# Optimization experiments

Measured on AMD Instinct MI355X. Metric: run time of the kernel, lower is better.

## Reference

```python
import jax, jax.numpy as jnp
import numpy as np

EPS = 0.1  # entropic regularization epsilon
N, F, R, H = 512, 32, 8, 128


def setup_inputs() -> dict:
    key = jax.random.key(0)
    ks = jax.random.split(key, 9)
    s0 = 1.0 / np.sqrt(F + R)
    sh = 1.0 / np.sqrt(H)
    return {
        "X": jax.random.normal(ks[0], (N, F), jnp.float32),
        "U": jax.random.normal(ks[1], (N, R), jnp.float32),
        "Y": jax.random.normal(ks[2], (N, R), jnp.float32),
        "Wx": jax.random.normal(ks[3], (F, H), jnp.float32) * s0,
        "Wy": jax.random.normal(ks[4], (R, H), jnp.float32) * s0,
        "b0": jnp.zeros((H,), jnp.float32),
        "W1": jax.random.normal(ks[5], (H, H), jnp.float32) * sh,
        "b1": jnp.zeros((H,), jnp.float32),
        "W2": jax.random.normal(ks[6], (H, H), jnp.float32) * sh,
        "b2": jnp.zeros((H,), jnp.float32),
        "Wout": jax.random.normal(ks[7], (H, 1), jnp.float32) * sh,
        "bout": jnp.zeros((1,), jnp.float32),
    }


def _mlp_tail(h, W1, b1, W2, b2, Wout, bout):
    h = jax.nn.softplus(h @ W1 + b1)
    h = jax.nn.softplus(h @ W2 + b2)
    return h @ Wout + bout  # [..., 1]


def reference(X, U, Y, Wx, Wy, b0, W1, b1, W2, b2, Wout, bout):
    n = X.shape[0]
    # ---- estimate_psi (potential net estimates 'y' side directly) ----
    h_row = jax.nn.softplus(X @ Wx + Y @ Wy + b0)              # [n, H]
    psi = _mlp_tail(h_row, W1, b1, W2, b2, Wout, bout)         # [n, 1]
    # ---- estimate_phi: entropic dual over all (X_i, Y_j) pairs ----
    # First-layer pre-activation built by broadcast-sum instead of concat.
    h_pair = jax.nn.softplus((X @ Wx)[:, None, :] + (Y @ Wy)[None, :, :] + b0)  # [n, n, H]
    psi_vals = _mlp_tail(h_pair, W1, b1, W2, b2, Wout, bout)[..., 0]            # [n, n]
    cost = U @ Y.T                                             # [n, n]
    slack = cost - psi_vals
    m = jnp.max(slack, axis=1, keepdims=True)                  # [n, 1]
    lme = jax.nn.logsumexp((slack - m) / EPS, axis=1, keepdims=True) \
          - jnp.log(jnp.asarray(n, slack.dtype)) + m / EPS
    phi = EPS * lme                                            # [n, 1]
    return jnp.mean(phi) + jnp.mean(psi)
```

## Files before the change

### kernel.cpp

```cpp
#include <hip/hip_runtime.h>
#include <hip/hip_bf16.h>
#include <math.h>

#define NN 512
#define HH 128
#define FF 32
#define RR 8
#define EPSV 0.1f
#define INV_EPS 10.0f
#define LOG2E 1.4426950408889634f
#define LN2 0.6931471805599453f
#define K2E (INV_EPS * LOG2E)

typedef unsigned short ushort_t;
typedef __attribute__((ext_vector_type(8))) short bf16x8;
typedef __attribute__((ext_vector_type(4))) float f32x4;
typedef __attribute__((ext_vector_type(4))) unsigned int u32x4;
typedef __attribute__((ext_vector_type(2))) unsigned int u32x2;

__device__ __forceinline__ float g2(float t) {
    return fmaxf(t, 0.f) + __log2f(1.f + __builtin_amdgcn_exp2f(-fabsf(t)));
}
__device__ __forceinline__ ushort_t f2b(float f) {
    unsigned u = __float_as_uint(f);
    return (ushort_t)((u + 0x7fffu + ((u >> 16) & 1u)) >> 16);
}
__device__ __forceinline__ float b2f(ushort_t h) {
    return __uint_as_float(((unsigned)h) << 16);
}
__device__ __forceinline__ unsigned pk2(float a, float b) {
    __hip_bfloat162 h = __float22bfloat162_rn(make_float2(a, b));
    return *reinterpret_cast<unsigned*>(&h);
}

__global__ __launch_bounds__(256) void prep_kernel(
    const float* __restrict__ X, const float* __restrict__ Y,
    const float* __restrict__ Wx, const float* __restrict__ Wy,
    const float* __restrict__ b0, const float* __restrict__ W1, const float* __restrict__ W2,
    const float* __restrict__ b1, const float* __restrict__ b2, const float* __restrict__ Wout,
    ushort_t* __restrict__ Wt1b, ushort_t* __restrict__ Wt2b,
    ushort_t* __restrict__ XWxb, ushort_t* __restrict__ YWyb,
    float* __restrict__ b1e, float* __restrict__ b2e, float* __restrict__ WoutE) {
    int gid = blockIdx.x * 256 + threadIdx.x;
    if (gid < 32768) {
        int sel = gid >> 14;
        int idx = gid & 16383;
        int n = idx >> 7, k = idx & 127;
        (sel ? Wt2b : Wt1b)[idx] = f2b((sel ? W2 : W1)[k * HH + n]);
    } else if (gid < 98304) {
        int g = gid - 32768;
        int i = g >> 7, h = g & 127;
        float s = b0[h];
#pragma unroll
        for (int f = 0; f < FF; ++f) s += X[i * FF + f] * Wx[f * HH + h];
        XWxb[g] = f2b(s * LOG2E);
    } else if (gid < 163840) {
        int g = gid - 98304;
        int i = g >> 7, h = g & 127;
        float s = 0.f;
#pragma unroll
        for (int r = 0; r < RR; ++r) s += Y[i * RR + r] * Wy[r * HH + h];
        YWyb[g] = f2b(s * LOG2E);
    } else if (gid < 163968) {
        b1e[gid - 163840] = b1[gid - 163840] * LOG2E;
    } else if (gid < 164096) {
        b2e[gid - 163968] = b2[gid - 163968] * LOG2E;
    } else if (gid < 164224) {
        WoutE[gid - 164096] = Wout[gid - 164096] * LN2;
    }
}

__device__ __forceinline__ void layer_flip(
    const ushort_t* __restrict__ Hin, const ushort_t* __restrict__ WtG,
    const float* __restrict__ bias, f32x4 acc[2][4], int r16, int g4, int wv) {
    const int hbase = wv * 32 + g4 * 4;
#pragma unroll
    for (int mt = 0; mt < 2; ++mt) {
        float4 bb = *(const float4*)&bias[hbase + mt * 16];
#pragma unroll
        for (int nt = 0; nt < 4; ++nt) {
            acc[mt][nt][0] = bb.x; acc[mt][nt][1] = bb.y;
            acc[mt][nt][2] = bb.z; acc[mt][nt][3] = bb.w;
        }
    }
    bf16x8 afr[2][4];
#pragma unroll
    for (int mt = 0; mt < 2; ++mt)
#pragma unroll
        for (int ks = 0; ks < 4; ++ks)
            afr[mt][ks] = *(const bf16x8*)&WtG[(wv * 32 + mt * 16 + r16) * HH + ks * 32 + g4 * 8];
#pragma unroll
    for (int ks = 0; ks < 4; ++ks) {
        const int kb = ks * 32 + g4 * 8;
#pragma unroll
        for (int nt = 0; nt < 4; ++nt) {
            const int j = nt * 16 + r16;
            bf16x8 bfr = *(const bf16x8*)&Hin[j * HH + (kb ^ ((j & 7) << 3))];
            acc[0][nt] = __builtin_amdgcn_mfma_f32_16x16x32_bf16(afr[0][ks], bfr, acc[0][nt], 0, 0, 0);
            acc[1][nt] = __builtin_amdgcn_mfma_f32_16x16x32_bf16(afr[1][ks], bfr, acc[1][nt], 0, 0, 0);
        }
    }
}

__global__ __launch_bounds__(256, 2) void pair_kernel(
    const ushort_t* __restrict__ XWxb, const ushort_t* __restrict__ YWyb,
    const ushort_t* __restrict__ Wt1b, const ushort_t* __restrict__ Wt2b,
    const float* __restrict__ U, const float* __restrict__ Y,
    const float* __restrict__ b1e, const float* __restrict__ b2e,
    const float* __restrict__ WoutE, const float* __restrict__ bout,
    float* __restrict__ psi_arr, float* __restrict__ Mp, float* __restrict__ Sp) {
    __shared__ ushort_t Hs0[64 * HH];
    __shared__ ushort_t Hs1[64 * HH];
    __shared__ float psum[4][64];

    const int i = blockIdx.x;
    const int half = blockIdx.y;
    const int t = threadIdx.x;
    const int wv = t >> 6;
    const int r16 = t & 15;
    const int g4 = (t >> 4) & 3;
    const int srow = t >> 4;
    const float boutv = bout[0];

    float axf[8];
    {
        bf16x8 axv = *(const bf16x8*)&XWxb[i * HH + r16 * 8];
#pragma unroll
        for (int e = 0; e < 8; ++e) axf[e] = b2f((ushort_t)axv[e]);
    }
    float costr[4];
    {
        const float4 u0 = *(const float4*)&U[i * RR];
        const float4 u1 = *(const float4*)&U[i * RR + 4];
#pragma unroll
        for (int c = 0; c < 4; ++c) {
            const int j = half * 256 + c * 64 + (t & 63);
            const float4 y0 = *(const float4*)&Y[j * RR];
            const float4 y1 = *(const float4*)&Y[j * RR + 4];
            costr[c] = u0.x * y0.x + u0.y * y0.y + u0.z * y0.z + u0.w * y0.w +
                       u1.x * y1.x + u1.y * y1.y + u1.z * y1.z + u1.w * y1.w;
        }
    }

    float m_l = -INFINITY, s_l = 0.f;
    f32x4 acc[2][4];
    bf16x8 pf[4];

#pragma unroll
    for (int s = 0; s < 4; ++s)
        pf[s] = *(const bf16x8*)&YWyb[(half * 256 + s * 16 + srow) * HH + r16 * 8];

#pragma unroll
    for (int c = 0; c < 4; ++c) {
        const int j0 = half * 256 + c * 64;
#pragma unroll
        for (int s = 0; s < 4; ++s) {
            const int p = s * 16 + srow;
            const bf16x8 yv = pf[s];
            unsigned pk[4];
#pragma unroll
            for (int e = 0; e < 4; ++e) {
                float v0 = g2(axf[2 * e]     + b2f((ushort_t)yv[2 * e]));
                float v1 = g2(axf[2 * e + 1] + b2f((ushort_t)yv[2 * e + 1]));
                pk[e] = pk2(v0, v1);
            }
            *(u32x4*)&Hs0[p * HH + ((r16 ^ (p & 7)) << 3)] = *(u32x4*)pk;
        }
        __syncthreads();
        if (c < 3) {
#pragma unroll
            for (int s = 0; s < 4; ++s)
                pf[s] = *(const bf16x8*)&YWyb[(j0 + 64 + s * 16 + srow) * HH + r16 * 8];
        }
        layer_flip(Hs0, Wt1b, b1e, acc, r16, g4, wv);
#pragma unroll
        for (int mt = 0; mt < 2; ++mt) {
            const int hb = wv * 32 + mt * 16 + g4 * 4;
#pragma unroll
            for (int nt = 0; nt < 4; ++nt) {
                const int j = nt * 16 + r16;
                u32x2 wv2;
                wv2[0] = pk2(g2(acc[mt][nt][0]), g2(acc[mt][nt][1]));
                wv2[1] = pk2(g2(acc[mt][nt][2]), g2(acc[mt][nt][3]));
                *(u32x2*)&Hs1[j * HH + (hb ^ ((j & 7) << 3))] = wv2;
            }
        }
        __syncthreads();
        layer_flip(Hs1, Wt2b, b2e, acc, r16, g4, wv);
        {
            float part[4] = {0.f, 0.f, 0.f, 0.f};
            const int hbase = wv * 32 + g4 * 4;
#pragma unroll
            for (int mt = 0; mt < 2; ++mt) {
                float4 wo = *(const float4*)&WoutE[hbase + mt * 16];
                const float wr[4] = {wo.x, wo.y, wo.z, wo.w};
#pragma unroll
                for (int r = 0; r < 4; ++r) {
                    const float wgt = wr[r];
#pragma unroll
                    for (int nt = 0; nt < 4; ++nt)
                        part[nt] += g2(acc[mt][nt][r]) * wgt;
                }
            }
#pragma unroll
            for (int nt = 0; nt < 4; ++nt) {
                part[nt] += __shfl_xor(part[nt], 16);
                part[nt] += __shfl_xor(part[nt], 32);
            }
            if (g4 == 0) {
#pragma unroll
                for (int nt = 0; nt < 4; ++nt) psum[wv][nt * 16 + r16] = part[nt];
            }
        }
        __syncthreads();
        if (t < 64) {
            const float psi = boutv + psum[0][t] + psum[1][t] + psum[2][t] + psum[3][t];
            const int j = j0 + t;
            const float sv = costr[c] - psi;
            const float mn = fmaxf(m_l, sv);
            s_l = s_l * __builtin_amdgcn_exp2f((m_l - mn) * K2E) +
                  __builtin_amdgcn_exp2f((sv - mn) * K2E);
            m_l = mn;
            if (j == i) psi_arr[i] = psi;
        }
    }
    if (t < 64) {
        float M = m_l;
#pragma unroll
        for (int o = 1; o < 64; o <<= 1) M = fmaxf(M, __shfl_xor(M, o));
        float S = s_l * __builtin_amdgcn_exp2f((m_l - M) * K2E);
#pragma unroll
        for (int o = 1; o < 64; o <<= 1) S += __shfl_xor(S, o);
        if (t == 0) {
            Mp[i * 2 + half] = M;
            Sp[i * 2 + half] = S;
        }
    }
}

__global__ __launch_bounds__(512) void finalize_kernel(
    const float* __restrict__ psi_arr, const float* __restrict__ Mp,
    const float* __restrict__ Sp, float* __restrict__ out) {
    __shared__ float red[8];
    const int t = threadIdx.x;
    const float M0 = Mp[2 * t], M1 = Mp[2 * t + 1];
    const float S0 = Sp[2 * t], S1 = Sp[2 * t + 1];
    const float Mg = fmaxf(M0, M1);
    const float S = S0 * __expf((M0 - Mg) * INV_EPS) + S1 * __expf((M1 - Mg) * INV_EPS);
    const float phi = EPSV * (__logf(S) - __logf((float)NN)) + Mg;
    float v = phi + psi_arr[t];
#pragma unroll
    for (int o = 1; o < 64; o <<= 1) v += __shfl_xor(v, o);
    if ((t & 63) == 0) red[t >> 6] = v;
    __syncthreads();
    if (t == 0) {
        float tot = 0.f;
#pragma unroll
        for (int w = 0; w < 8; ++w) tot += red[w];
        out[0] = tot / (float)NN;
    }
}

extern "C" void kernel_launch(void* const* d_in, const int* in_sizes, int n_in,
                              void* d_out, int out_size, void* d_ws, size_t ws_size,
                              hipStream_t stream) {
    (void)in_sizes; (void)n_in; (void)out_size; (void)ws_size;
    const float* X    = (const float*)d_in[0];
    const float* U    = (const float*)d_in[1];
    const float* Y    = (const float*)d_in[2];
    const float* Wx   = (const float*)d_in[3];
    const float* Wy   = (const float*)d_in[4];
    const float* b0   = (const float*)d_in[5];
    const float* W1   = (const float*)d_in[6];
    const float* b1   = (const float*)d_in[7];
    const float* W2   = (const float*)d_in[8];
    const float* b2   = (const float*)d_in[9];
    const float* Wout = (const float*)d_in[10];
    const float* bout = (const float*)d_in[11];
    float* out = (float*)d_out;

    char* ws = (char*)d_ws;
    ushort_t* Wt1b    = (ushort_t*)(ws);
    ushort_t* Wt2b    = (ushort_t*)(ws + 32768);
    ushort_t* XWxb    = (ushort_t*)(ws + 65536);
    ushort_t* YWyb    = (ushort_t*)(ws + 196608);
    float*    psi_arr = (float*)(ws + 327680);
    float*    Mp      = (float*)(ws + 329728);
    float*    Sp      = (float*)(ws + 333824);
    float*    b1e     = (float*)(ws + 337920);
    float*    b2e     = (float*)(ws + 338432);
    float*    WoutE   = (float*)(ws + 338944);

    prep_kernel<<<642, 256, 0, stream>>>(X, Y, Wx, Wy, b0, W1, W2, b1, b2, Wout,
                                         Wt1b, Wt2b, XWxb, YWyb, b1e, b2e, WoutE);
    pair_kernel<<<dim3(NN, 2), 256, 0, stream>>>(XWxb, YWyb, Wt1b, Wt2b, U, Y,
                                                 b1e, b2e, WoutE, bout, psi_arr, Mp, Sp);
    finalize_kernel<<<1, 512, 0, stream>>>(psi_arr, Mp, Sp, out);
}
```

Before: 60.75 us.

## Repartition second MLP layer per wave to drop a block barrier per chunk

The second hidden layer is remapped so each wave computes all 128 outputs for its own 16 pair rows. The output projection and the online logsumexp update can then be reduced inside the wave, which removes the shared psum buffer and one __syncthreads per 64-pair chunk. The final max/sum combine now runs across the four waves through a small shared array. First-layer weight fragments and bias are hoisted into registers once per block, and staging of the next chunk moves to the end of the loop. In exchange, each wave now re-reads all of the second-layer weights from global or cache every chunk, and register pressure goes up.

```diff
diff --git a/kernel.cpp b/kernel.cpp
--- a/kernel.cpp
+++ b/kernel.cpp
@@ -70,38 +70,6 @@
     }
 }
 
-__device__ __forceinline__ void layer_flip(
-    const ushort_t* __restrict__ Hin, const ushort_t* __restrict__ WtG,
-    const float* __restrict__ bias, f32x4 acc[2][4], int r16, int g4, int wv) {
-    const int hbase = wv * 32 + g4 * 4;
-#pragma unroll
-    for (int mt = 0; mt < 2; ++mt) {
-        float4 bb = *(const float4*)&bias[hbase + mt * 16];
-#pragma unroll
-        for (int nt = 0; nt < 4; ++nt) {
-            acc[mt][nt][0] = bb.x; acc[mt][nt][1] = bb.y;
-            acc[mt][nt][2] = bb.z; acc[mt][nt][3] = bb.w;
-        }
-    }
-    bf16x8 afr[2][4];
-#pragma unroll
-    for (int mt = 0; mt < 2; ++mt)
-#pragma unroll
-        for (int ks = 0; ks < 4; ++ks)
-            afr[mt][ks] = *(const bf16x8*)&WtG[(wv * 32 + mt * 16 + r16) * HH + ks * 32 + g4 * 8];
-#pragma unroll
-    for (int ks = 0; ks < 4; ++ks) {
-        const int kb = ks * 32 + g4 * 8;
-#pragma unroll
-        for (int nt = 0; nt < 4; ++nt) {
-            const int j = nt * 16 + r16;
-            bf16x8 bfr = *(const bf16x8*)&Hin[j * HH + (kb ^ ((j & 7) << 3))];
-            acc[0][nt] = __builtin_amdgcn_mfma_f32_16x16x32_bf16(afr[0][ks], bfr, acc[0][nt], 0, 0, 0);
-            acc[1][nt] = __builtin_amdgcn_mfma_f32_16x16x32_bf16(afr[1][ks], bfr, acc[1][nt], 0, 0, 0);
-        }
-    }
-}
-
 __global__ __launch_bounds__(256, 2) void pair_kernel(
     const ushort_t* __restrict__ XWxb, const ushort_t* __restrict__ YWyb,
     const ushort_t* __restrict__ Wt1b, const ushort_t* __restrict__ Wt2b,
@@ -111,7 +79,7 @@
     float* __restrict__ psi_arr, float* __restrict__ Mp, float* __restrict__ Sp) {
     __shared__ ushort_t Hs0[64 * HH];
     __shared__ ushort_t Hs1[64 * HH];
-    __shared__ float psum[4][64];
+    __shared__ float redMS[8];
 
     const int i = blockIdx.x;
     const int half = blockIdx.y;
@@ -120,6 +88,7 @@
     const int r16 = t & 15;
     const int g4 = (t >> 4) & 3;
     const int srow = t >> 4;
+    const int jl = wv * 16 + r16;
     const float boutv = bout[0];
 
     float axf[8];
@@ -134,25 +103,27 @@
         const float4 u1 = *(const float4*)&U[i * RR + 4];
 #pragma unroll
         for (int c = 0; c < 4; ++c) {
-            const int j = half * 256 + c * 64 + (t & 63);
+            const int j = half * 256 + c * 64 + jl;
             const float4 y0 = *(const float4*)&Y[j * RR];
             const float4 y1 = *(const float4*)&Y[j * RR + 4];
             costr[c] = u0.x * y0.x + u0.y * y0.y + u0.z * y0.z + u0.w * y0.w +
                        u1.x * y1.x + u1.y * y1.y + u1.z * y1.z + u1.w * y1.w;
         }
     }
+    bf16x8 afr1[2][4];
+#pragma unroll
+    for (int mt = 0; mt < 2; ++mt)
+#pragma unroll
+        for (int ks = 0; ks < 4; ++ks)
+            afr1[mt][ks] = *(const bf16x8*)&Wt1b[(wv * 32 + mt * 16 + r16) * HH + ks * 32 + g4 * 8];
+    float4 bias1h[2];
+    bias1h[0] = *(const float4*)&b1e[wv * 32 + g4 * 4];
+    bias1h[1] = *(const float4*)&b1e[wv * 32 + 16 + g4 * 4];
 
     float m_l = -INFINITY, s_l = 0.f;
-    f32x4 acc[2][4];
     bf16x8 pf[4];
 
-#pragma unroll
-    for (int s = 0; s < 4; ++s)
-        pf[s] = *(const bf16x8*)&YWyb[(half * 256 + s * 16 + srow) * HH + r16 * 8];
-
-#pragma unroll
-    for (int c = 0; c < 4; ++c) {
-        const int j0 = half * 256 + c * 64;
+    auto stage = [&](ushort_t* dst) {
 #pragma unroll
         for (int s = 0; s < 4; ++s) {
             const int p = s * 16 + srow;
@@ -164,15 +135,43 @@
                 float v1 = g2(axf[2 * e + 1] + b2f((ushort_t)yv[2 * e + 1]));
                 pk[e] = pk2(v0, v1);
             }
-            *(u32x4*)&Hs0[p * HH + ((r16 ^ (p & 7)) << 3)] = *(u32x4*)pk;
-        }
-        __syncthreads();
+            *(u32x4*)&dst[p * HH + ((r16 ^ (p & 7)) << 3)] = *(u32x4*)pk;
+        }
+    };
+
+#pragma unroll
+    for (int s = 0; s < 4; ++s)
+        pf[s] = *(const bf16x8*)&YWyb[(half * 256 + s * 16 + srow) * HH + r16 * 8];
+    stage(Hs0);
+    __syncthreads();
+
+#pragma unroll
+    for (int c = 0; c < 4; ++c) {
+        const int j0 = half * 256 + c * 64;
         if (c < 3) {
 #pragma unroll
             for (int s = 0; s < 4; ++s)
                 pf[s] = *(const bf16x8*)&YWyb[(j0 + 64 + s * 16 + srow) * HH + r16 * 8];
         }
-        layer_flip(Hs0, Wt1b, b1e, acc, r16, g4, wv);
+        f32x4 acc[2][4];
+#pragma unroll
+        for (int mt = 0; mt < 2; ++mt)
+#pragma unroll
+            for (int nt = 0; nt < 4; ++nt) {
+                acc[mt][nt][0] = bias1h[mt].x; acc[mt][nt][1] = bias1h[mt].y;
+                acc[mt][nt][2] = bias1h[mt].z; acc[mt][nt][3] = bias1h[mt].w;
+            }
+#pragma unroll
+        for (int ks = 0; ks < 4; ++ks) {
+            const int kb = ks * 32 + g4 * 8;
+#pragma unroll
+            for (int nt = 0; nt < 4; ++nt) {
+                const int j = nt * 16 + r16;
+                bf16x8 bfr = *(const bf16x8*)&Hs0[j * HH + (kb ^ ((j & 7) << 3))];
+                acc[0][nt] = __builtin_amdgcn_mfma_f32_16x16x32_bf16(afr1[0][ks], bfr, acc[0][nt], 0, 0, 0);
+                acc[1][nt] = __builtin_amdgcn_mfma_f32_16x16x32_bf16(afr1[1][ks], bfr, acc[1][nt], 0, 0, 0);
+            }
+        }
 #pragma unroll
         for (int mt = 0; mt < 2; ++mt) {
             const int hb = wv * 32 + mt * 16 + g4 * 4;
@@ -186,55 +185,67 @@
             }
         }
         __syncthreads();
-        layer_flip(Hs1, Wt2b, b2e, acc, r16, g4, wv);
         {
-            float part[4] = {0.f, 0.f, 0.f, 0.f};
-            const int hbase = wv * 32 + g4 * 4;
-#pragma unroll
-            for (int mt = 0; mt < 2; ++mt) {
-                float4 wo = *(const float4*)&WoutE[hbase + mt * 16];
-                const float wr[4] = {wo.x, wo.y, wo.z, wo.w};
-#pragma unroll
-                for (int r = 0; r < 4; ++r) {
-                    const float wgt = wr[r];
-#pragma unroll
-                    for (int nt = 0; nt < 4; ++nt)
-                        part[nt] += g2(acc[mt][nt][r]) * wgt;
+            bf16x8 b2r[4];
+#pragma unroll
+            for (int ks = 0; ks < 4; ++ks)
+                b2r[ks] = *(const bf16x8*)&Hs1[jl * HH + ((ks * 32 + g4 * 8) ^ ((jl & 7) << 3))];
+            f32x4 acc2[8];
+#pragma unroll
+            for (int mt = 0; mt < 8; ++mt) {
+                float4 bb = *(const float4*)&b2e[mt * 16 + g4 * 4];
+                acc2[mt][0] = bb.x; acc2[mt][1] = bb.y; acc2[mt][2] = bb.z; acc2[mt][3] = bb.w;
+            }
+#pragma unroll
+            for (int ks = 0; ks < 4; ++ks)
+#pragma unroll
+                for (int mt = 0; mt < 8; ++mt) {
+                    bf16x8 afr2 = *(const bf16x8*)&Wt2b[(mt * 16 + r16) * HH + ks * 32 + g4 * 8];
+                    acc2[mt] = __builtin_amdgcn_mfma_f32_16x16x32_bf16(afr2, b2r[ks], acc2[mt], 0, 0, 0);
                 }
-            }
-#pragma unroll
-            for (int nt = 0; nt < 4; ++nt) {
-                part[nt] += __shfl_xor(part[nt], 16);
-                part[nt] += __shfl_xor(part[nt], 32);
-            }
+            float part = 0.f;
+#pragma unroll
+            for (int mt = 0; mt < 8; ++mt) {
+                float4 wo = *(const float4*)&WoutE[mt * 16 + g4 * 4];
+                part += g2(acc2[mt][0]) * wo.x + g2(acc2[mt][1]) * wo.y +
+                        g2(acc2[mt][2]) * wo.z + g2(acc2[mt][3]) * wo.w;
+            }
+            part += __shfl_xor(part, 16);
+            part += __shfl_xor(part, 32);
             if (g4 == 0) {
-#pragma unroll
-                for (int nt = 0; nt < 4; ++nt) psum[wv][nt * 16 + r16] = part[nt];
-            }
-        }
-        __syncthreads();
-        if (t < 64) {
-            const float psi = boutv + psum[0][t] + psum[1][t] + psum[2][t] + psum[3][t];
-            const int j = j0 + t;
-            const float sv = costr[c] - psi;
-            const float mn = fmaxf(m_l, sv);
-            s_l = s_l * __builtin_amdgcn_exp2f((m_l - mn) * K2E) +
-                  __builtin_amdgcn_exp2f((sv - mn) * K2E);
-            m_l = mn;
-            if (j == i) psi_arr[i] = psi;
-        }
-    }
-    if (t < 64) {
-        float M = m_l;
-#pragma unroll
-        for (int o = 1; o < 64; o <<= 1) M = fmaxf(M, __shfl_xor(M, o));
-        float S = s_l * __builtin_amdgcn_exp2f((m_l - M) * K2E);
-#pragma unroll
-        for (int o = 1; o < 64; o <<= 1) S += __shfl_xor(S, o);
-        if (t == 0) {
-            Mp[i * 2 + half] = M;
-            Sp[i * 2 + half] = S;
-        }
+                const float psi = part + boutv;
+                const int j = j0 + jl;
+                if (j == i) psi_arr[i] = psi;
+                const float sv = costr[c] - psi;
+                const float mn = fmaxf(m_l, sv);
+                s_l = s_l * __builtin_amdgcn_exp2f((m_l - mn) * K2E) +
+                      __builtin_amdgcn_exp2f((sv - mn) * K2E);
+                m_l = mn;
+            }
+        }
+        if (c < 3) {
+            stage(Hs0);
+            __syncthreads();
+        }
+    }
+    float M = m_l;
+#pragma unroll
+    for (int o = 1; o < 64; o <<= 1) M = fmaxf(M, __shfl_xor(M, o));
+    float S = s_l * __builtin_amdgcn_exp2f((m_l - M) * K2E);
+#pragma unroll
+    for (int o = 1; o < 64; o <<= 1) S += __shfl_xor(S, o);
+    if ((t & 63) == 0) { redMS[wv * 2] = M; redMS[wv * 2 + 1] = S; }
+    __syncthreads();
+    if (t == 0) {
+        float Mg = redMS[0];
+#pragma unroll
+        for (int q = 1; q < 4; ++q) Mg = fmaxf(Mg, redMS[q * 2]);
+        float S2 = 0.f;
+#pragma unroll
+        for (int q = 0; q < 4; ++q)
+            S2 += redMS[q * 2 + 1] * __builtin_amdgcn_exp2f((redMS[q * 2] - Mg) * K2E);
+        Mp[i * 2 + half] = Mg;
+        Sp[i * 2 + half] = S2;
     }
 }
 
```

Result: slower. 95.29 us (+56.9%).
